# Optimization experiments

Measured on AMD Instinct MI355X. Metric: run time of the kernel, lower is better.

The kernel has to match this reference:

```python
import jax, jax.numpy as jnp
import numpy as np

H = 512      # hidden_size
NH = 8       # num_heads
DH = H // NH # head_dim = 64
NL = 2       # num_layers
R = 64       # number of AST relation types
PAD = 0      # padding relation index
FF = 4 * H   # FFN inner dim
B, T, S = 4, 512, 512
NEG = -1e10
EPS = 1e-5


def layer_norm(x, g, b):
    m = jnp.mean(x, axis=-1, keepdims=True)
    v = jnp.mean((x - m) ** 2, axis=-1, keepdims=True)
    return (x - m) * jax.lax.rsqrt(v + EPS) * g + b


def setup_inputs() -> dict:
    key = jax.random.key(0)
    ks = iter(jax.random.split(key, 40))

    def n(shape, scale=0.02):
        return jax.random.normal(next(ks), shape, dtype=jnp.float32) * scale

    inp = {
        'q': jax.random.normal(next(ks), (B, T, H), dtype=jnp.float32),
        'kv': jax.random.normal(next(ks), (B, S, H), dtype=jnp.float32),
        'rel_emb_k': n((R, DH)).at[PAD].set(0.0),
        'rel_emb_v': n((R, DH)).at[PAD].set(0.0),
        'Wq_s': n((NL, H, H)), 'bq_s': jnp.zeros((NL, H)),
        'Wk_s': n((NL, H, H)), 'Wv_s': n((NL, H, H)),
        'Wo_s': n((NL, H, H)), 'bo_s': jnp.zeros((NL, H)),
        'ln1_g': jnp.ones((NL, H)), 'ln1_b': jnp.zeros((NL, H)),
        'Wq_c': n((NL, H, H)), 'bq_c': jnp.zeros((NL, H)),
        'Wk_c': n((NL, H, H)), 'Wv_c': n((NL, H, H)),
        'Wo_c': n((NL, H, H)), 'bo_c': jnp.zeros((NL, H)),
        'ln2_g': jnp.ones((NL, H)), 'ln2_b': jnp.zeros((NL, H)),
        'W1': n((NL, H, FF)), 'b1': jnp.zeros((NL, FF)),
        'W2': n((NL, FF, H)), 'b2': jnp.zeros((NL, H)),
        'ln3_g': jnp.ones((NL, H)), 'ln3_b': jnp.zeros((NL, H)),
        'rel_ids': jax.random.randint(next(ks), (B, T, T), 0, R),
        'enc_mask': jnp.ones((B, S), dtype=bool),
    }
    return inp


def reference(q, kv, rel_emb_k, rel_emb_v,
              Wq_s, bq_s, Wk_s, Wv_s, Wo_s, bo_s, ln1_g, ln1_b,
              Wq_c, bq_c, Wk_c, Wv_c, Wo_c, bo_c, ln2_g, ln2_b,
              W1, b1, W2, b2, ln3_g, ln3_b,
              rel_ids, enc_mask):
    scale = np.sqrt(DH).astype(np.float32)
    # relation embeddings shared across layers/heads: [B,T,T,DH]
    rel_k = rel_emb_k[rel_ids]
    rel_v = rel_emb_v[rel_ids]
    tril = jnp.tril(jnp.ones((T, T), dtype=bool))
    rel_mask = (rel_ids != PAD) & tril[None]

    o = q
    for i in range(NL):
        # --- relation-aware masked self-attention ---
        Q = (o @ Wq_s[i] + bq_s[i]).reshape(B, T, NH, DH)
        K = (o @ Wk_s[i]).reshape(B, T, NH, DH)
        V = (o @ Wv_s[i]).reshape(B, T, NH, DH)
        # Q . (K + rel_k)^T decomposed to avoid materializing [B,NH,T,T,DH]
        e = (jnp.einsum('blhd,bmhd->bhlm', Q, K)
             + jnp.einsum('blhd,blmd->bhlm', Q, rel_k)) / scale
        e = jnp.where(rel_mask[:, None], e, NEG)
        a = jax.nn.softmax(e, axis=-1)
        att = (jnp.einsum('bhlm,bmhd->blhd', a, V)
               + jnp.einsum('bhlm,blmd->blhd', a, rel_v)).reshape(B, T, H)
        o = layer_norm(o + att @ Wo_s[i] + bo_s[i], ln1_g[i], ln1_b[i])

        # --- cross-attention ---
        Qc = (o @ Wq_c[i] + bq_c[i]).reshape(B, T, NH, DH)
        Kc = (kv @ Wk_c[i]).reshape(B, S, NH, DH)
        Vc = (kv @ Wv_c[i]).reshape(B, S, NH, DH)
        ec = jnp.einsum('bthd,bshd->bhts', Qc, Kc) / scale
        ec = jnp.where(enc_mask[:, None, None, :], ec, NEG)
        ac = jax.nn.softmax(ec, axis=-1)
        oc = jnp.einsum('bhts,bshd->bthd', ac, Vc).reshape(B, T, H)
        o = layer_norm(o + oc @ Wo_c[i] + bo_c[i], ln2_g[i], ln2_b[i])

        # --- feedforward ---
        h = jax.nn.relu(o @ W1[i] + b1[i])
        o = layer_norm(o + h @ W2[i] + b2[i], ln3_g[i], ln3_b[i])
    return o
```

## Files before the change

kernel.cpp:

```cpp
#include <hip/hip_runtime.h>

static constexpr int Hc  = 512;
static constexpr int NHc = 8;
static constexpr int DHc = 64;
static constexpr int NLc = 2;
static constexpr int Rc  = 64;
static constexpr int FFc = 2048;
static constexpr int Bc  = 4;
static constexpr int Tc  = 512;
#define NEGV (-1e10f)
#define EPSV 1e-5f
#define THRV 6.0f

typedef unsigned short u16;
typedef unsigned char u8;
typedef __attribute__((ext_vector_type(8))) short s16x8;
typedef __attribute__((ext_vector_type(4))) float f32x4;

__device__ __forceinline__ f32x4 mfma_bf16(s16x8 a, s16x8 b, f32x4 c) {
  return __builtin_amdgcn_mfma_f32_16x16x32_bf16(a, b, c, 0, 0, 0);
}
__device__ __forceinline__ u16 f2bf(float f) {
  union { float f; unsigned u; } x; x.f = f;
  unsigned r = (x.u + 0x7FFFu + ((x.u >> 16) & 1u)) >> 16;
  return (u16)r;
}
__device__ __forceinline__ float bf2f(u16 h) {
  union { unsigned u; float f; } x; x.u = ((unsigned)h) << 16;
  return x.f;
}
__device__ __forceinline__ unsigned cvtpk(float a, float b) {
  unsigned r;
  asm("v_cvt_pk_bf16_f32 %0, %1, %2" : "=v"(r) : "v"(a), "v"(b));
  return r;
}

template <int BM, int BN, bool RELU, int OUT>
__global__ __launch_bounds__(256) void gemm_mfma(
    const u16* __restrict__ A, const u16* __restrict__ Wt,
    const float* __restrict__ bias, int biasN,
    void* __restrict__ Cout, int N, int K) {
  __shared__ u16 As[BM * 32];
  __shared__ u16 Bs[BN * 32];
  const int tid = threadIdx.x;
  const int w = tid >> 6, lane = tid & 63, g = lane >> 4, li = lane & 15;
  const int bn = blockIdx.x * BN, bm = blockIdx.y * BM;
  const int r0 = (w & 1) * (BM / 2), c0 = (w >> 1) * (BN / 2);
  constexpr int MR = BM / 32, NR = BN / 32;
  constexpr int AIT = BM / 64, BIT = BN / 64;
  f32x4 acc[MR][NR];
#pragma unroll
  for (int i = 0; i < MR; ++i)
#pragma unroll
    for (int j = 0; j < NR; ++j) acc[i][j] = (f32x4){0.f, 0.f, 0.f, 0.f};

  s16x8 va[AIT], vb[BIT];
#pragma unroll
  for (int it = 0; it < AIT; ++it) {
    int s = it * 256 + tid, row = s >> 2, ch = s & 3;
    va[it] = *(const s16x8*)(A + (size_t)(bm + row) * K + ch * 8);
  }
#pragma unroll
  for (int it = 0; it < BIT; ++it) {
    int s = it * 256 + tid, row = s >> 2, ch = s & 3;
    vb[it] = *(const s16x8*)(Wt + (size_t)(bn + row) * K + ch * 8);
  }

  for (int k0 = 0; k0 < K; k0 += 32) {
    __syncthreads();
#pragma unroll
    for (int it = 0; it < AIT; ++it) {
      int s = it * 256 + tid, row = s >> 2, ch = s & 3;
      *(s16x8*)&As[row * 32 + ((ch ^ (row & 3)) * 8)] = va[it];
    }
#pragma unroll
    for (int it = 0; it < BIT; ++it) {
      int s = it * 256 + tid, row = s >> 2, ch = s & 3;
      *(s16x8*)&Bs[row * 32 + ((ch ^ (row & 3)) * 8)] = vb[it];
    }
    if (k0 + 32 < K) {
#pragma unroll
      for (int it = 0; it < AIT; ++it) {
        int s = it * 256 + tid, row = s >> 2, ch = s & 3;
        va[it] = *(const s16x8*)(A + (size_t)(bm + row) * K + k0 + 32 + ch * 8);
      }
#pragma unroll
      for (int it = 0; it < BIT; ++it) {
        int s = it * 256 + tid, row = s >> 2, ch = s & 3;
        vb[it] = *(const s16x8*)(Wt + (size_t)(bn + row) * K + k0 + 32 + ch * 8);
      }
    }
    __syncthreads();
    s16x8 ar[MR], br[NR];
#pragma unroll
    for (int i = 0; i < MR; ++i) {
      int row = r0 + i * 16 + li;
      ar[i] = *(const s16x8*)&As[row * 32 + ((g ^ (row & 3)) * 8)];
    }
#pragma unroll
    for (int j = 0; j < NR; ++j) {
      int row = c0 + j * 16 + li;
      br[j] = *(const s16x8*)&Bs[row * 32 + ((g ^ (row & 3)) * 8)];
    }
#pragma unroll
    for (int i = 0; i < MR; ++i)
#pragma unroll
      for (int j = 0; j < NR; ++j) acc[i][j] = mfma_bf16(ar[i], br[j], acc[i][j]);
  }

#pragma unroll
  for (int j = 0; j < NR; ++j) {
    int col = bn + c0 + j * 16 + li;
    float bv = (bias && col < biasN) ? bias[col] : 0.f;
#pragma unroll
    for (int i = 0; i < MR; ++i) {
#pragma unroll
      for (int r = 0; r < 4; ++r) {
        int rowg = bm + r0 + i * 16 + 4 * g + r;
        float v = acc[i][j][r] + bv;
        if (RELU) v = fmaxf(v, 0.f);
        if (OUT == 0) ((float*)Cout)[(size_t)rowg * N + col] = v;
        else          ((u16*)Cout)[(size_t)rowg * N + col] = f2bf(v);
      }
    }
  }
}

struct WPtrs { const float* p[10]; };

__global__ __launch_bounds__(256) void wcvt(WPtrs wp, u16* __restrict__ dst) {
  constexpr int NE = 20;
  constexpr int srcIdx[NE] = {0,1,0,1,3,3,4,4,5,5,6,6,7,7,2,2,8,8,9,9};
  constexpr int srcOff[NE] = {0,0,262144,262144,0,262144,0,262144,0,262144,
                              0,262144,0,262144,0,262144,0,1048576,0,1048576};
  constexpr int dstOff[NE] = {0,262144,524288,786432,1048576,1310720,
                              1572864,1835008,2097152,2359296,2621440,2883584,
                              3145728,3407872,3670016,3932160,
                              4194304,5242880,6291456,7340032};
  constexpr int KsA[NE] = {512,512,512,512,512,512,512,512,512,512,
                           512,512,512,512,512,512,512,512,2048,2048};
  constexpr int NsA[NE] = {512,512,512,512,512,512,512,512,512,512,
                           512,512,512,512,512,512,2048,2048,512,512};
  constexpr int tileStart[NE] = {0,64,128,192,256,320,384,448,512,576,
                                 640,704,768,832,896,960,1024,1280,1536,1792};
  __shared__ float ts[64 * 65];
  const int tid = threadIdx.x;
  const int bid = blockIdx.x;
  int e = 0;
#pragma unroll
  for (int i = 1; i < NE; ++i) if (bid >= tileStart[i]) e = i;
  const int t = bid - tileStart[e];
  const int Ks_ = KsA[e], Ns_ = NsA[e];
  const int tn = t % (Ns_ >> 6), tk = t / (Ns_ >> 6);
  const float* src = wp.p[srcIdx[e]] + srcOff[e];

  {
    int r = tid >> 2, cb = (tid & 3) * 16;
    const float* sp = src + (size_t)(tk * 64 + r) * Ns_ + tn * 64 + cb;
#pragma unroll
    for (int j = 0; j < 4; ++j) {
      float4 v = ((const float4*)sp)[j];
      float* d = &ts[r * 65 + cb + j * 4];
      d[0] = v.x; d[1] = v.y; d[2] = v.z; d[3] = v.w;
    }
  }
  __syncthreads();
  {
    int n = tid >> 2, kb = (tid & 3) * 16;
    u16* dp = dst + dstOff[e] + (size_t)(tn * 64 + n) * Ks_ + tk * 64 + kb;
    s16x8 o0, o1;
#pragma unroll
    for (int j = 0; j < 8; ++j) o0[j] = (short)f2bf(ts[(kb + j) * 65 + n]);
#pragma unroll
    for (int j = 0; j < 8; ++j) o1[j] = (short)f2bf(ts[(kb + 8 + j) * 65 + n]);
    *(s16x8*)dp = o0;
    *(s16x8*)(dp + 8) = o1;
  }
}

__global__ __launch_bounds__(256) void acvt(
    const float* __restrict__ q, const float* __restrict__ kv,
    const float* __restrict__ relv, const int* __restrict__ rel,
    u16* __restrict__ obf, u16* __restrict__ kvbf, u16* __restrict__ relvt,
    u8* __restrict__ rel8) {
  int bid = blockIdx.x, tid = threadIdx.x;
  if (bid >= 1025) {
    size_t i = (size_t)(bid - 1025) * 2048 + (size_t)tid * 8;
    int4 a = *(const int4*)(rel + i);
    int4 b = *(const int4*)(rel + i + 4);
    unsigned lo = (unsigned)(a.x & 255) | ((unsigned)(a.y & 255) << 8) |
                  ((unsigned)(a.z & 255) << 16) | ((unsigned)(a.w & 255) << 24);
    unsigned hi = (unsigned)(b.x & 255) | ((unsigned)(b.y & 255) << 8) |
                  ((unsigned)(b.z & 255) << 16) | ((unsigned)(b.w & 255) << 24);
    *(uint2*)(rel8 + i) = make_uint2(lo, hi);
    return;
  }
  if (bid == 1024) {
    int d = tid >> 2, rb = (tid & 3) * 16;
    s16x8 o0, o1;
#pragma unroll
    for (int j = 0; j < 8; ++j) o0[j] = (short)f2bf(relv[(rb + j) * 64 + d]);
#pragma unroll
    for (int j = 0; j < 8; ++j) o1[j] = (short)f2bf(relv[(rb + 8 + j) * 64 + d]);
    *(s16x8*)(relvt + d * 64 + rb) = o0;
    *(s16x8*)(relvt + d * 64 + rb + 8) = o1;
    return;
  }
  int i = bid * 256 + tid;
  const float* src; u16* dst; size_t off;
  if (i < 131072) { src = q; dst = obf; off = (size_t)i * 8; }
  else { src = kv; dst = kvbf; off = (size_t)(i - 131072) * 8; }
  float4 a = *(const float4*)(src + off);
  float4 b = *(const float4*)(src + off + 4);
  s16x8 o;
  o[0] = (short)f2bf(a.x); o[1] = (short)f2bf(a.y);
  o[2] = (short)f2bf(a.z); o[3] = (short)f2bf(a.w);
  o[4] = (short)f2bf(b.x); o[5] = (short)f2bf(b.y);
  o[6] = (short)f2bf(b.z); o[7] = (short)f2bf(b.w);
  *(s16x8*)(dst + off) = o;
}

__global__ __launch_bounds__(256) void qr_kernel(
    const u16* __restrict__ Q, const float* __restrict__ relk,
    u16* __restrict__ Qr) {
  __shared__ float rk[64 * 65];
  __shared__ float qs[4][64];
  const int tid = threadIdx.x;
  {
    int r = tid >> 2, cb = (tid & 3) * 16;
    const float* sp = relk + r * 64 + cb;
#pragma unroll
    for (int j = 0; j < 4; ++j) {
      float4 v = ((const float4*)sp)[j];
      float* d = &rk[r * 65 + cb + j * 4];
      d[0] = v.x; d[1] = v.y; d[2] = v.z; d[3] = v.w;
    }
  }
  const int sub = tid >> 6, r = tid & 63;
  const int unit = blockIdx.x * 4 + sub;
  qs[sub][r] = bf2f(Q[(size_t)(unit >> 3) * 1024 + (unit & 7) * 64 + r]);
  __syncthreads();
  float acc = 0.f;
#pragma unroll
  for (int d = 0; d < 64; ++d) acc += qs[sub][d] * rk[r * 65 + d];
  Qr[(size_t)unit * 64 + r] = f2bf(acc);
}

#define LOADKREL(KF, RF, C8) do {                                              \
    _Pragma("unroll") for (int mt = 0; mt < 4; ++mt) {                         \
      KF[mt * 2 + 0] = *(const s16x8*)(kp + (size_t)(C8) * 65536 + mt * 16384);\
      KF[mt * 2 + 1] = *(const s16x8*)(kp + (size_t)(C8) * 65536 + mt * 16384 + 32); \
      RF[mt] = *(const unsigned*)(rp8 + (C8) * 64 + mt * 16);                  \
    } } while (0)

#define COMPUTE_SELF(KF, RF, C8) do {                                          \
    s16x8 vf[8];                                                               \
    _Pragma("unroll") for (int df = 0; df < 4; ++df) {                         \
      vf[df * 2 + 0] = *(const s16x8*)(vp + (size_t)(C8) * 64 + df * 32768);   \
      vf[df * 2 + 1] = *(const s16x8*)(vp + (size_t)(C8) * 64 + df * 32768 + 32); } \
    f32x4 sf[4];                                                               \
    _Pragma("unroll") for (int mt = 0; mt < 4; ++mt) {                         \
      sf[mt] = (f32x4){0.f, 0.f, 0.f, 0.f};                                    \
      sf[mt] = mfma_bf16(KF[mt * 2 + 0], aq0, sf[mt]);                         \
      sf[mt] = mfma_bf16(KF[mt * 2 + 1], aq1, sf[mt]); }                       \
    float p[4][4];                                                             \
    int rl[4][4];                                                              \
    float pmax = NEGV;                                                         \
    _Pragma("unroll") for (int mt = 0; mt < 4; ++mt) {                         \
      _Pragma("unroll") for (int r = 0; r < 4; ++r) {                          \
        int rel = (int)((RF[mt] >> (8 * r)) & 255u);                           \
        rl[mt][r] = rel;                                                       \
        bool valid = (rel != 0) && ((C8) * 64 + mt * 16 + 4 * g + r <= lrow);  \
        p[mt][r] = valid ? (sf[mt][r] + qrs[li * 66 + rel]) * 0.125f : NEGV;   \
        pmax = fmaxf(pmax, p[mt][r]); } }                                      \
    pmax = fmaxf(pmax, __shfl_xor(pmax, 16));                                  \
    pmax = fmaxf(pmax, __shfl_xor(pmax, 32));                                  \
    if (__any(pmax > mrow + THRV)) {                                           \
      float mnew = (pmax > mrow + THRV) ? pmax : mrow;                         \
      float f = __expf(mrow - mnew);                                           \
      rsum *= f;                                                               \
      _Pragma("unroll") for (int j = 0; j < 8; ++j) {                          \
        float2* p2 = (float2*)&bk[li * 66 + g * 16 + 2 * j];                   \
        float2 v = *p2; v.x *= f; v.y *= f; *p2 = v; }                         \
      _Pragma("unroll") for (int r = 0; r < 4; ++r) {                          \
        float fr = __shfl(f, 4 * g + r);                                       \
        _Pragma("unroll") for (int df = 0; df < 4; ++df) oacc[df][r] *= fr; }  \
      mrow = mnew; }                                                           \
    unsigned pk[4][2];                                                         \
    _Pragma("unroll") for (int mt = 0; mt < 4; ++mt) {                         \
      _Pragma("unroll") for (int r = 0; r < 4; ++r) {                          \
        float pv = __expf(p[mt][r] - mrow);                                    \
        p[mt][r] = pv;                                                         \
        rsum += pv;                                                            \
        if (pv > 0.f) atomicAdd(&bk[li * 66 + rl[mt][r]], pv); }               \
      pk[mt][0] = cvtpk(p[mt][0], p[mt][1]);                                   \
      pk[mt][1] = cvtpk(p[mt][2], p[mt][3]); }                                 \
    _Pragma("unroll") for (int kk = 0; kk < 2; ++kk) {                         \
      union { s16x8 v; unsigned u[4]; } pa;                                    \
      _Pragma("unroll") for (int q = 0; q < 4; ++q) {                          \
        int src = ((2 * (g & 1) + (q >> 1)) << 4) + li;                        \
        unsigned uA = __shfl(pk[2 * kk][q & 1], src);                          \
        unsigned uB = __shfl(pk[2 * kk + 1][q & 1], src);                      \
        pa.u[q] = (g < 2) ? uA : uB; }                                         \
      _Pragma("unroll") for (int df = 0; df < 4; ++df)                         \
        oacc[df] = mfma_bf16(pa.v, vf[df * 2 + kk], oacc[df]); }               \
  } while (0)

__global__ __launch_bounds__(64) void attn_self_part(
    const u16* __restrict__ Qb, const u16* __restrict__ Kb,
    const u16* __restrict__ VT,
    const u16* __restrict__ Qrb, const u8* __restrict__ rel8,
    const u16* __restrict__ relvt,
    float* __restrict__ po, float2* __restrict__ pms) {
  __shared__ float qrs[16 * 66];
  __shared__ float buck[16 * 66];
  float* bk = buck;

  const int lane = threadIdx.x;
  const int g = lane >> 4, li = lane & 15;
  const int qt = blockIdx.x, h = blockIdx.y;
  const int b = blockIdx.z >> 2, s = blockIdx.z & 3;
  const int lrow = qt * 16 + li;
  const int growq = b * 512 + qt * 16;

  const u16* qp = Qb + (size_t)(growq + li) * 1024 + h * 64;
  s16x8 aq0 = *(const s16x8*)(qp + g * 8);
  s16x8 aq1 = *(const s16x8*)(qp + 32 + g * 8);
  const u16* kp = Kb + (size_t)(b * 512 + li) * 1024 + h * 64 + g * 8;
  const u16* vp = VT + (size_t)(h * 64 + li) * 2048 + b * 512 + g * 8;
  const u8* rp8 = rel8 + (size_t)(growq + li) * 512 + 4 * g;

  {
    int row = lane >> 2, c16 = (lane & 3) * 16;
    const u16* qrp = Qrb + ((size_t)(growq + row) * 8 + h) * 64 + c16;
    s16x8 v0 = *(const s16x8*)qrp;
    s16x8 v1 = *(const s16x8*)(qrp + 8);
#pragma unroll
    for (int j = 0; j < 8; ++j) {
      qrs[row * 66 + c16 + j] = bf2f((u16)v0[j]);
      qrs[row * 66 + c16 + 8 + j] = bf2f((u16)v1[j]);
    }
#pragma unroll
    for (int j = 0; j < 5; ++j) {
      int fid = j * 64 + lane;
      if (fid < 264) *(float4*)&buck[fid * 4] = make_float4(0.f, 0.f, 0.f, 0.f);
    }
  }

  float mrow = NEGV, rsum = 0.f;
  f32x4 oacc[4];
#pragma unroll
  for (int d = 0; d < 4; ++d) oacc[d] = (f32x4){0.f, 0.f, 0.f, 0.f};

  s16x8 kA[8], kB[8];
  unsigned rA[4], rB[4];
  LOADKREL(kA, rA, 2 * s);
  LOADKREL(kB, rB, 2 * s + 1);
  COMPUTE_SELF(kA, rA, 2 * s);
  COMPUTE_SELF(kB, rB, 2 * s + 1);

  rsum += __shfl_xor(rsum, 16);
  rsum += __shfl_xor(rsum, 32);

#pragma unroll
  for (int kk = 0; kk < 2; ++kk) {
    float bb[8];
#pragma unroll
    for (int j = 0; j < 4; ++j) {
      float2 v = *(const float2*)&bk[li * 66 + kk * 32 + g * 8 + 2 * j];
      bb[2 * j] = v.x; bb[2 * j + 1] = v.y;
    }
    union { s16x8 v; unsigned u[4]; } pb;
#pragma unroll
    for (int q = 0; q < 4; ++q) pb.u[q] = cvtpk(bb[2 * q], bb[2 * q + 1]);
#pragma unroll
    for (int df = 0; df < 4; ++df) {
      s16x8 rb = *(const s16x8*)(relvt + (df * 16 + li) * 64 + kk * 32 + g * 8);
      oacc[df] = mfma_bf16(pb.v, rb, oacc[df]);
    }
  }

  const size_t idx = (size_t)(b * 8 + h) * 512 + qt * 16;
#pragma unroll
  for (int df = 0; df < 4; ++df)
#pragma unroll
    for (int r = 0; r < 4; ++r)
      po[((idx + 4 * g + r) * 4 + s) * 64 + df * 16 + li] = oacc[df][r];
  if (lane < 16) pms[(idx + lane) * 4 + s] = make_float2(mrow, rsum);
}

#define LOADK_X(KF, C8) do {                                                   \
    _Pragma("unroll") for (int mt = 0; mt < 4; ++mt) {                         \
      KF[mt * 2 + 0] = *(const s16x8*)(kp + (size_t)(C8) * 65536 + mt * 16384);\
      KF[mt * 2 + 1] = *(const s16x8*)(kp + (size_t)(C8) * 65536 + mt * 16384 + 32); \
    } } while (0)

#define COMPUTE_X(KF, C8) do {                                                 \
    s16x8 vf[8];                                                               \
    _Pragma("unroll") for (int df = 0; df < 4; ++df) {                         \
      vf[df * 2 + 0] = *(const s16x8*)(vp + (size_t)(C8) * 64 + df * 32768);   \
      vf[df * 2 + 1] = *(const s16x8*)(vp + (size_t)(C8) * 64 + df * 32768 + 32); } \
    f32x4 sf[4];                                                               \
    _Pragma("unroll") for (int mt = 0; mt < 4; ++mt) {                         \
      sf[mt] = (f32x4){0.f, 0.f, 0.f, 0.f};                                    \
      sf[mt] = mfma_bf16(KF[mt * 2 + 0], aq0, sf[mt]);                         \
      sf[mt] = mfma_bf16(KF[mt * 2 + 1], aq1, sf[mt]); }                       \
    float p[4][4];                                                             \
    float pmax = NEGV;                                                         \
    _Pragma("unroll") for (int mt = 0; mt < 4; ++mt)                           \
      _Pragma("unroll") for (int r = 0; r < 4; ++r) {                          \
        p[mt][r] = sf[mt][r] * 0.125f;                                         \
        pmax = fmaxf(pmax, p[mt][r]); }                                        \
    pmax = fmaxf(pmax, __shfl_xor(pmax, 16));                                  \
    pmax = fmaxf(pmax, __shfl_xor(pmax, 32));                                  \
    if (__any(pmax > mrow + THRV)) {                                           \
      float mnew = (pmax > mrow + THRV) ? pmax : mrow;                         \
      float f = __expf(mrow - mnew);                                           \
      rsum *= f;                                                               \
      _Pragma("unroll") for (int r = 0; r < 4; ++r) {                          \
        float fr = __shfl(f, 4 * g + r);                                       \
        _Pragma("unroll") for (int df = 0; df < 4; ++df) oacc[df][r] *= fr; }  \
      mrow = mnew; }                                                           \
    unsigned pk[4][2];                                                         \
    _Pragma("unroll") for (int mt = 0; mt < 4; ++mt) {                         \
      _Pragma("unroll") for (int r = 0; r < 4; ++r) {                          \
        float pv = __expf(p[mt][r] - mrow);                                    \
        p[mt][r] = pv;                                                         \
        rsum += pv; }                                                          \
      pk[mt][0] = cvtpk(p[mt][0], p[mt][1]);                                   \
      pk[mt][1] = cvtpk(p[mt][2], p[mt][3]); }                                 \
    _Pragma("unroll") for (int kk = 0; kk < 2; ++kk) {                         \
      union { s16x8 v; unsigned u[4]; } pa;                                    \
      _Pragma("unroll") for (int q = 0; q < 4; ++q) {                          \
        int src = ((2 * (g & 1) + (q >> 1)) << 4) + li;                        \
        unsigned uA = __shfl(pk[2 * kk][q & 1], src);                          \
        unsigned uB = __shfl(pk[2 * kk + 1][q & 1], src);                      \
        pa.u[q] = (g < 2) ? uA : uB; }                                         \
      _Pragma("unroll") for (int df = 0; df < 4; ++df)                         \
        oacc[df] = mfma_bf16(pa.v, vf[df * 2 + kk], oacc[df]); }               \
  } while (0)

__global__ __launch_bounds__(64) void attn_cross_part(
    const u16* __restrict__ Qb,
    const u16* __restrict__ Kb,
    const u16* __restrict__ VT,
    float* __restrict__ po, float2* __restrict__ pms) {
  const int lane = threadIdx.x;
  const int g = lane >> 4, li = lane & 15;
  const int qt = blockIdx.x, h = blockIdx.y;
  const int b = blockIdx.z >> 2, s = blockIdx.z & 3;
  const int growq = b * 512 + qt * 16;

  const u16* qp = Qb + (size_t)(growq + li) * 512 + h * 64;
  s16x8 aq0 = *(const s16x8*)(qp + g * 8);
  s16x8 aq1 = *(const s16x8*)(qp + 32 + g * 8);
  const u16* kp = Kb + (size_t)(b * 512 + li) * 1024 + h * 64 + g * 8;
  const u16* vp = VT + (size_t)(h * 64 + li) * 2048 + b * 512 + g * 8;

  float mrow = NEGV, rsum = 0.f;
  f32x4 oacc[4];
#pragma unroll
  for (int d = 0; d < 4; ++d) oacc[d] = (f32x4){0.f, 0.f, 0.f, 0.f};

  s16x8 kA[8], kB[8];
  LOADK_X(kA, 2 * s);
  LOADK_X(kB, 2 * s + 1);
  COMPUTE_X(kA, 2 * s);
  COMPUTE_X(kB, 2 * s + 1);

  rsum += __shfl_xor(rsum, 16);
  rsum += __shfl_xor(rsum, 32);

  const size_t idx = (size_t)(b * 8 + h) * 512 + qt * 16;
#pragma unroll
  for (int df = 0; df < 4; ++df)
#pragma unroll
    for (int r = 0; r < 4; ++r)
      po[((idx + 4 * g + r) * 4 + s) * 64 + df * 16 + li] = oacc[df][r];
  if (lane < 16) pms[(idx + lane) * 4 + s] = make_float2(mrow, rsum);
}

__global__ __launch_bounds__(256) void attn_merge(
    const float* __restrict__ po, const float2* __restrict__ pms,
    u16* __restrict__ att) {
  const int t = threadIdx.x;
  const size_t idx = (size_t)blockIdx.x * 16 + (t >> 4);
  const int d4 = (t & 15) * 4;
  float2 ms[4];
  float m = NEGV;
#pragma unroll
  for (int s = 0; s < 4; ++s) {
    ms[s] = pms[idx * 4 + s];
    m = fmaxf(m, ms[s].x);
  }
  float rs = 0.f;
  float4 o = make_float4(0.f, 0.f, 0.f, 0.f);
#pragma unroll
  for (int s = 0; s < 4; ++s) {
    float f = __expf(ms[s].x - m);
    rs += f * ms[s].y;
    float4 v = *(const float4*)(po + (idx * 4 + s) * 64 + d4);
    o.x += f * v.x; o.y += f * v.y; o.z += f * v.z; o.w += f * v.w;
  }
  const float inv = 1.f / rs;
  const int b = (int)(idx >> 12), h = (int)(idx >> 9) & 7, row = (int)(idx & 511);
  ushort4 ov;
  ov.x = f2bf(o.x * inv);
  ov.y = f2bf(o.y * inv);
  ov.z = f2bf(o.z * inv);
  ov.w = f2bf(o.w * inv);
  *(ushort4*)(att + (size_t)(b * 512 + row) * 512 + h * 64 + d4) = ov;
}

__global__ __launch_bounds__(256) void ln_res(
    const float* __restrict__ x, const float* __restrict__ dlt,
    const float* __restrict__ g, const float* __restrict__ bta,
    float* __restrict__ out, u16* __restrict__ obf) {
  __shared__ float red_s[256];
  const int row = blockIdx.x, tid = threadIdx.x;
  const size_t base = (size_t)row * Hc;
  float v0 = x[base + tid] + dlt[base + tid];
  float v1 = x[base + tid + 256] + dlt[base + tid + 256];

  red_s[tid] = v0 + v1;
  __syncthreads();
  for (int s = 128; s > 0; s >>= 1) {
    if (tid < s) red_s[tid] += red_s[tid + s];
    __syncthreads();
  }
  const float mean = red_s[0] * (1.f / Hc);
  __syncthreads();
  const float d0 = v0 - mean, d1 = v1 - mean;
  red_s[tid] = d0 * d0 + d1 * d1;
  __syncthreads();
  for (int s = 128; s > 0; s >>= 1) {
    if (tid < s) red_s[tid] += red_s[tid + s];
    __syncthreads();
  }
  const float rstd = rsqrtf(red_s[0] * (1.f / Hc) + EPSV);
  float o0 = d0 * rstd * g[tid] + bta[tid];
  float o1 = d1 * rstd * g[tid + 256] + bta[tid + 256];
  out[base + tid] = o0;
  out[base + tid + 256] = o1;
  obf[base + tid] = f2bf(o0);
  obf[base + tid + 256] = f2bf(o1);
}

extern "C" void kernel_launch(void* const* d_in, const int* in_sizes, int n_in,
                              void* d_out, int out_size, void* d_ws, size_t ws_size,
                              hipStream_t stream) {
  const float* q    = (const float*)d_in[0];
  const float* kv   = (const float*)d_in[1];
  const float* relk = (const float*)d_in[2];
  const float* relv = (const float*)d_in[3];
  const float* Wq_s = (const float*)d_in[4];
  const float* bq_s = (const float*)d_in[5];
  const float* Wk_s = (const float*)d_in[6];
  const float* Wv_s = (const float*)d_in[7];
  const float* Wo_s = (const float*)d_in[8];
  const float* bo_s = (const float*)d_in[9];
  const float* ln1g = (const float*)d_in[10];
  const float* ln1b = (const float*)d_in[11];
  const float* Wq_c = (const float*)d_in[12];
  const float* bq_c = (const float*)d_in[13];
  const float* Wk_c = (const float*)d_in[14];
  const float* Wv_c = (const float*)d_in[15];
  const float* Wo_c = (const float*)d_in[16];
  const float* bo_c = (const float*)d_in[17];
  const float* ln2g = (const float*)d_in[18];
  const float* ln2b = (const float*)d_in[19];
  const float* W1   = (const float*)d_in[20];
  const float* b1   = (const float*)d_in[21];
  const float* W2   = (const float*)d_in[22];
  const float* b2   = (const float*)d_in[23];
  const float* ln3g = (const float*)d_in[24];
  const float* ln3b = (const float*)d_in[25];
  const int*   rel  = (const int*)d_in[26];

  char* wsb = (char*)d_ws;
  const size_t NT = (size_t)Bc * Tc;
  float* o     = (float*)wsb;  wsb += NT * Hc * 4;
  float* bDlt  = (float*)wsb;  wsb += NT * Hc * 4;
  u16* Qr      = (u16*)wsb;    wsb += NT * 8 * 64 * 2;
  u16* obf     = (u16*)wsb;    wsb += NT * Hc * 2;
  u16* kvbf    = (u16*)wsb;    wsb += NT * Hc * 2;
  u16* bQK     = (u16*)wsb;    wsb += NT * 1024 * 2;
  u16* bVt     = (u16*)wsb;    wsb += (size_t)512 * 2048 * 2;
  u16* bQc     = (u16*)wsb;    wsb += NT * Hc * 2;
  u16* bKc     = (u16*)wsb;    wsb += NT * 1024 * 2;
  u16* bVtc    = (u16*)wsb;    wsb += (size_t)1024 * 2048 * 2;
  u16* bAtt    = (u16*)wsb;    wsb += NT * Hc * 2;
  u16* bH      = (u16*)wsb;    wsb += NT * FFc * 2;
  u16* relvt   = (u16*)wsb;    wsb += 64 * 64 * 2;
  u8* rel8     = (u8*)wsb;     wsb += (size_t)NT * 512;
  u16* wbuf    = (u16*)wsb;    wsb += (size_t)8388608 * 2;
  float* po    = (float*)wsb;  wsb += (size_t)16384 * 4 * 64 * 4;
  float2* pms  = (float2*)wsb; wsb += (size_t)16384 * 4 * 8;

  WPtrs wp;
  wp.p[0] = Wq_s; wp.p[1] = Wk_s; wp.p[2] = Wv_s; wp.p[3] = Wo_s;
  wp.p[4] = Wq_c; wp.p[5] = Wk_c; wp.p[6] = Wv_c; wp.p[7] = Wo_c;
  wp.p[8] = W1;   wp.p[9] = W2;

  dim3 blk(256);
  wcvt<<<dim3(2048), blk, 0, stream>>>(wp, wbuf);
  acvt<<<dim3(1537), blk, 0, stream>>>(q, kv, relv, rel, obf, kvbf, relvt, rel8);
  hipMemcpyAsync(o, q, NT * Hc * 4, hipMemcpyDeviceToDevice, stream);

  gemm_mfma<64, 128, false, 1><<<dim3(8, 32), blk, 0, stream>>>(
      kvbf, wbuf + 2097152, nullptr, 0, bKc, 1024, 512);
  gemm_mfma<64, 128, false, 1><<<dim3(16, 16), blk, 0, stream>>>(
      wbuf + 2621440, kvbf, nullptr, 0, bVtc, 2048, 512);

  const dim3 gLN(NT);
  const dim3 gPART(32, 8, 16);
  const dim3 gMERGE(1024);
  for (int i = 0; i < NLc; ++i) {
    gemm_mfma<64, 128, false, 1><<<dim3(8, 32), blk, 0, stream>>>(
        obf, wbuf + (size_t)i * 524288, bq_s + i * Hc, Hc, bQK, 1024, 512);
    gemm_mfma<64, 64, false, 1><<<dim3(32, 8), blk, 0, stream>>>(
        wbuf + 3670016 + (size_t)i * 262144, obf, nullptr, 0, bVt, 2048, 512);
    qr_kernel<<<dim3(4096), blk, 0, stream>>>(bQK, relk, Qr);
    attn_self_part<<<gPART, dim3(64), 0, stream>>>(
        bQK, bQK + 512, bVt, Qr, rel8, relvt, po, pms);
    attn_merge<<<gMERGE, blk, 0, stream>>>(po, pms, bAtt);
    gemm_mfma<64, 64, false, 0><<<dim3(8, 32), blk, 0, stream>>>(
        bAtt, wbuf + 1048576 + (size_t)i * 262144, bo_s + i * Hc, Hc, bDlt, Hc, 512);
    ln_res<<<gLN, blk, 0, stream>>>(o, bDlt, ln1g + i * Hc, ln1b + i * Hc, o, obf);

    gemm_mfma<64, 64, false, 1><<<dim3(8, 32), blk, 0, stream>>>(
        obf, wbuf + 1572864 + (size_t)i * 262144, bq_c + i * Hc, Hc, bQc, Hc, 512);
    attn_cross_part<<<gPART, dim3(64), 0, stream>>>(
        bQc, bKc + i * 512, bVtc + (size_t)i * 512 * 2048, po, pms);
    attn_merge<<<gMERGE, blk, 0, stream>>>(po, pms, bAtt);
    gemm_mfma<64, 64, false, 0><<<dim3(8, 32), blk, 0, stream>>>(
        bAtt, wbuf + 3145728 + (size_t)i * 262144, bo_c + i * Hc, Hc, bDlt, Hc, 512);
    ln_res<<<gLN, blk, 0, stream>>>(o, bDlt, ln2g + i * Hc, ln2b + i * Hc, o, obf);

    gemm_mfma<64, 128, true, 1><<<dim3(16, 32), blk, 0, stream>>>(
        obf, wbuf + 4194304 + (size_t)i * 1048576, b1 + i * FFc, FFc, bH, FFc, 512);
    gemm_mfma<64, 64, false, 0><<<dim3(8, 32), blk, 0, stream>>>(
        bH, wbuf + 6291456 + (size_t)i * 1048576, b2 + i * Hc, Hc, bDlt, Hc, 2048);
    float* lnout = (i == NLc - 1) ? (float*)d_out : o;
    ln_res<<<gLN, blk, 0, stream>>>(o, bDlt, ln3g + i * Hc, ln3b + i * Hc, lnout, obf);
  }
}
```

Before: 389.4 us.

## Replace split-K flash attention with materialized score, softmax, and PV kernels

Replaces the fused online-softmax attention kernels (split across four key chunks with a merge pass) with three separate kernels: an MFMA score GEMM that writes bf16 scores to global memory, a row-wise softmax kernel that also builds the relation-value bucket sums, and a PV GEMM that folds the relation bucket in as extra K columns. The q-to-o fp32 copy is also fused into the input conversion kernel instead of using a separate memcpy. This removes the lazy-rescale logic, the per-element LDS atomics inside the MFMA loop, and the partial-result merge, at the cost of writing and reading full score and probability matrices through HBM and storing scores in bf16 before softmax.

```diff
diff --git a/kernel.cpp b/kernel.cpp
--- a/kernel.cpp
+++ b/kernel.cpp
@@ -10,7 +10,6 @@
 static constexpr int Tc  = 512;
 #define NEGV (-1e10f)
 #define EPSV 1e-5f
-#define THRV 6.0f
 
 typedef unsigned short u16;
 typedef unsigned char u8;
@@ -28,11 +27,6 @@
 __device__ __forceinline__ float bf2f(u16 h) {
   union { unsigned u; float f; } x; x.u = ((unsigned)h) << 16;
   return x.f;
-}
-__device__ __forceinline__ unsigned cvtpk(float a, float b) {
-  unsigned r;
-  asm("v_cvt_pk_bf16_f32 %0, %1, %2" : "=v"(r) : "v"(a), "v"(b));
-  return r;
 }
 
 template <int BM, int BN, bool RELU, int OUT>
@@ -182,7 +176,7 @@
     const float* __restrict__ q, const float* __restrict__ kv,
     const float* __restrict__ relv, const int* __restrict__ rel,
     u16* __restrict__ obf, u16* __restrict__ kvbf, u16* __restrict__ relvt,
-    u8* __restrict__ rel8) {
+    u8* __restrict__ rel8, float* __restrict__ ocp) {
   int bid = blockIdx.x, tid = threadIdx.x;
   if (bid >= 1025) {
     size_t i = (size_t)(bid - 1025) * 2048 + (size_t)tid * 8;
@@ -208,10 +202,15 @@
   }
   int i = bid * 256 + tid;
   const float* src; u16* dst; size_t off;
-  if (i < 131072) { src = q; dst = obf; off = (size_t)i * 8; }
+  bool isq = (i < 131072);
+  if (isq) { src = q; dst = obf; off = (size_t)i * 8; }
   else { src = kv; dst = kvbf; off = (size_t)(i - 131072) * 8; }
   float4 a = *(const float4*)(src + off);
   float4 b = *(const float4*)(src + off + 4);
+  if (isq) {
+    *(float4*)(ocp + off) = a;
+    *(float4*)(ocp + off + 4) = b;
+  }
   s16x8 o;
   o[0] = (short)f2bf(a.x); o[1] = (short)f2bf(a.y);
   o[2] = (short)f2bf(a.z); o[3] = (short)f2bf(a.w);
@@ -246,270 +245,181 @@
   Qr[(size_t)unit * 64 + r] = f2bf(acc);
 }
 
-#define LOADKREL(KF, RF, C8) do {                                              \
-    _Pragma("unroll") for (int mt = 0; mt < 4; ++mt) {                         \
-      KF[mt * 2 + 0] = *(const s16x8*)(kp + (size_t)(C8) * 65536 + mt * 16384);\
-      KF[mt * 2 + 1] = *(const s16x8*)(kp + (size_t)(C8) * 65536 + mt * 16384 + 32); \
-      RF[mt] = *(const unsigned*)(rp8 + (C8) * 64 + mt * 16);                  \
-    } } while (0)
-
-#define COMPUTE_SELF(KF, RF, C8) do {                                          \
-    s16x8 vf[8];                                                               \
-    _Pragma("unroll") for (int df = 0; df < 4; ++df) {                         \
-      vf[df * 2 + 0] = *(const s16x8*)(vp + (size_t)(C8) * 64 + df * 32768);   \
-      vf[df * 2 + 1] = *(const s16x8*)(vp + (size_t)(C8) * 64 + df * 32768 + 32); } \
-    f32x4 sf[4];                                                               \
-    _Pragma("unroll") for (int mt = 0; mt < 4; ++mt) {                         \
-      sf[mt] = (f32x4){0.f, 0.f, 0.f, 0.f};                                    \
-      sf[mt] = mfma_bf16(KF[mt * 2 + 0], aq0, sf[mt]);                         \
-      sf[mt] = mfma_bf16(KF[mt * 2 + 1], aq1, sf[mt]); }                       \
-    float p[4][4];                                                             \
-    int rl[4][4];                                                              \
-    float pmax = NEGV;                                                         \
-    _Pragma("unroll") for (int mt = 0; mt < 4; ++mt) {                         \
-      _Pragma("unroll") for (int r = 0; r < 4; ++r) {                          \
-        int rel = (int)((RF[mt] >> (8 * r)) & 255u);                           \
-        rl[mt][r] = rel;                                                       \
-        bool valid = (rel != 0) && ((C8) * 64 + mt * 16 + 4 * g + r <= lrow);  \
-        p[mt][r] = valid ? (sf[mt][r] + qrs[li * 66 + rel]) * 0.125f : NEGV;   \
-        pmax = fmaxf(pmax, p[mt][r]); } }                                      \
-    pmax = fmaxf(pmax, __shfl_xor(pmax, 16));                                  \
-    pmax = fmaxf(pmax, __shfl_xor(pmax, 32));                                  \
-    if (__any(pmax > mrow + THRV)) {                                           \
-      float mnew = (pmax > mrow + THRV) ? pmax : mrow;                         \
-      float f = __expf(mrow - mnew);                                           \
-      rsum *= f;                                                               \
-      _Pragma("unroll") for (int j = 0; j < 8; ++j) {                          \
-        float2* p2 = (float2*)&bk[li * 66 + g * 16 + 2 * j];                   \
-        float2 v = *p2; v.x *= f; v.y *= f; *p2 = v; }                         \
-      _Pragma("unroll") for (int r = 0; r < 4; ++r) {                          \
-        float fr = __shfl(f, 4 * g + r);                                       \
-        _Pragma("unroll") for (int df = 0; df < 4; ++df) oacc[df][r] *= fr; }  \
-      mrow = mnew; }                                                           \
-    unsigned pk[4][2];                                                         \
-    _Pragma("unroll") for (int mt = 0; mt < 4; ++mt) {                         \
-      _Pragma("unroll") for (int r = 0; r < 4; ++r) {                          \
-        float pv = __expf(p[mt][r] - mrow);                                    \
-        p[mt][r] = pv;                                                         \
-        rsum += pv;                                                            \
-        if (pv > 0.f) atomicAdd(&bk[li * 66 + rl[mt][r]], pv); }               \
-      pk[mt][0] = cvtpk(p[mt][0], p[mt][1]);                                   \
-      pk[mt][1] = cvtpk(p[mt][2], p[mt][3]); }                                 \
-    _Pragma("unroll") for (int kk = 0; kk < 2; ++kk) {                         \
-      union { s16x8 v; unsigned u[4]; } pa;                                    \
-      _Pragma("unroll") for (int q = 0; q < 4; ++q) {                          \
-        int src = ((2 * (g & 1) + (q >> 1)) << 4) + li;                        \
-        unsigned uA = __shfl(pk[2 * kk][q & 1], src);                          \
-        unsigned uB = __shfl(pk[2 * kk + 1][q & 1], src);                      \
-        pa.u[q] = (g < 2) ? uA : uB; }                                         \
-      _Pragma("unroll") for (int df = 0; df < 4; ++df)                         \
-        oacc[df] = mfma_bf16(pa.v, vf[df * 2 + kk], oacc[df]); }               \
-  } while (0)
-
-__global__ __launch_bounds__(64) void attn_self_part(
-    const u16* __restrict__ Qb, const u16* __restrict__ Kb,
-    const u16* __restrict__ VT,
-    const u16* __restrict__ Qrb, const u8* __restrict__ rel8,
-    const u16* __restrict__ relvt,
-    float* __restrict__ po, float2* __restrict__ pms) {
-  __shared__ float qrs[16 * 66];
-  __shared__ float buck[16 * 66];
-  float* bk = buck;
-
-  const int lane = threadIdx.x;
-  const int g = lane >> 4, li = lane & 15;
-  const int qt = blockIdx.x, h = blockIdx.y;
-  const int b = blockIdx.z >> 2, s = blockIdx.z & 3;
-  const int lrow = qt * 16 + li;
-  const int growq = b * 512 + qt * 16;
-
-  const u16* qp = Qb + (size_t)(growq + li) * 1024 + h * 64;
-  s16x8 aq0 = *(const s16x8*)(qp + g * 8);
-  s16x8 aq1 = *(const s16x8*)(qp + 32 + g * 8);
-  const u16* kp = Kb + (size_t)(b * 512 + li) * 1024 + h * 64 + g * 8;
-  const u16* vp = VT + (size_t)(h * 64 + li) * 2048 + b * 512 + g * 8;
-  const u8* rp8 = rel8 + (size_t)(growq + li) * 512 + 4 * g;
-
-  {
-    int row = lane >> 2, c16 = (lane & 3) * 16;
-    const u16* qrp = Qrb + ((size_t)(growq + row) * 8 + h) * 64 + c16;
-    s16x8 v0 = *(const s16x8*)qrp;
-    s16x8 v1 = *(const s16x8*)(qrp + 8);
-#pragma unroll
-    for (int j = 0; j < 8; ++j) {
-      qrs[row * 66 + c16 + j] = bf2f((u16)v0[j]);
-      qrs[row * 66 + c16 + 8 + j] = bf2f((u16)v1[j]);
-    }
-#pragma unroll
-    for (int j = 0; j < 5; ++j) {
-      int fid = j * 64 + lane;
-      if (fid < 264) *(float4*)&buck[fid * 4] = make_float4(0.f, 0.f, 0.f, 0.f);
-    }
-  }
-
-  float mrow = NEGV, rsum = 0.f;
-  f32x4 oacc[4];
-#pragma unroll
-  for (int d = 0; d < 4; ++d) oacc[d] = (f32x4){0.f, 0.f, 0.f, 0.f};
-
-  s16x8 kA[8], kB[8];
-  unsigned rA[4], rB[4];
-  LOADKREL(kA, rA, 2 * s);
-  LOADKREL(kB, rB, 2 * s + 1);
-  COMPUTE_SELF(kA, rA, 2 * s);
-  COMPUTE_SELF(kB, rB, 2 * s + 1);
-
-  rsum += __shfl_xor(rsum, 16);
-  rsum += __shfl_xor(rsum, 32);
-
-#pragma unroll
-  for (int kk = 0; kk < 2; ++kk) {
-    float bb[8];
+__global__ __launch_bounds__(256) void attn_score(
+    const u16* __restrict__ Qb, int qstride,
+    const u16* __restrict__ Kb, int kstride,
+    u16* __restrict__ S) {
+  const int tid = threadIdx.x;
+  const int w = tid >> 6, lane = tid & 63, g = lane >> 4, li = lane & 15;
+  const int mt = blockIdx.x, lt = blockIdx.y, bh = blockIdx.z;
+  const int b = bh >> 3, h = bh & 7;
+  const int lbase = lt * 128 + (w & 1) * 64;
+  const int mbase = mt * 128 + (w >> 1) * 64;
+
+  s16x8 aq[4][2], bk[4][2];
+#pragma unroll
+  for (int i = 0; i < 4; ++i) {
+    const u16* qp = Qb + (size_t)(b * 512 + lbase + i * 16 + li) * qstride + h * 64;
+    aq[i][0] = *(const s16x8*)(qp + g * 8);
+    aq[i][1] = *(const s16x8*)(qp + 32 + g * 8);
+  }
+#pragma unroll
+  for (int j = 0; j < 4; ++j) {
+    const u16* kp = Kb + (size_t)(b * 512 + mbase + j * 16 + li) * kstride + h * 64;
+    bk[j][0] = *(const s16x8*)(kp + g * 8);
+    bk[j][1] = *(const s16x8*)(kp + 32 + g * 8);
+  }
+  f32x4 acc[4][4];
+#pragma unroll
+  for (int i = 0; i < 4; ++i)
 #pragma unroll
     for (int j = 0; j < 4; ++j) {
-      float2 v = *(const float2*)&bk[li * 66 + kk * 32 + g * 8 + 2 * j];
-      bb[2 * j] = v.x; bb[2 * j + 1] = v.y;
-    }
-    union { s16x8 v; unsigned u[4]; } pb;
-#pragma unroll
-    for (int q = 0; q < 4; ++q) pb.u[q] = cvtpk(bb[2 * q], bb[2 * q + 1]);
-#pragma unroll
-    for (int df = 0; df < 4; ++df) {
-      s16x8 rb = *(const s16x8*)(relvt + (df * 16 + li) * 64 + kk * 32 + g * 8);
-      oacc[df] = mfma_bf16(pb.v, rb, oacc[df]);
-    }
-  }
-
-  const size_t idx = (size_t)(b * 8 + h) * 512 + qt * 16;
-#pragma unroll
-  for (int df = 0; df < 4; ++df)
-#pragma unroll
-    for (int r = 0; r < 4; ++r)
-      po[((idx + 4 * g + r) * 4 + s) * 64 + df * 16 + li] = oacc[df][r];
-  if (lane < 16) pms[(idx + lane) * 4 + s] = make_float2(mrow, rsum);
-}
-
-#define LOADK_X(KF, C8) do {                                                   \
-    _Pragma("unroll") for (int mt = 0; mt < 4; ++mt) {                         \
-      KF[mt * 2 + 0] = *(const s16x8*)(kp + (size_t)(C8) * 65536 + mt * 16384);\
-      KF[mt * 2 + 1] = *(const s16x8*)(kp + (size_t)(C8) * 65536 + mt * 16384 + 32); \
-    } } while (0)
-
-#define COMPUTE_X(KF, C8) do {                                                 \
-    s16x8 vf[8];                                                               \
-    _Pragma("unroll") for (int df = 0; df < 4; ++df) {                         \
-      vf[df * 2 + 0] = *(const s16x8*)(vp + (size_t)(C8) * 64 + df * 32768);   \
-      vf[df * 2 + 1] = *(const s16x8*)(vp + (size_t)(C8) * 64 + df * 32768 + 32); } \
-    f32x4 sf[4];                                                               \
-    _Pragma("unroll") for (int mt = 0; mt < 4; ++mt) {                         \
-      sf[mt] = (f32x4){0.f, 0.f, 0.f, 0.f};                                    \
-      sf[mt] = mfma_bf16(KF[mt * 2 + 0], aq0, sf[mt]);                         \
-      sf[mt] = mfma_bf16(KF[mt * 2 + 1], aq1, sf[mt]); }                       \
-    float p[4][4];                                                             \
-    float pmax = NEGV;                                                         \
-    _Pragma("unroll") for (int mt = 0; mt < 4; ++mt)                           \
-      _Pragma("unroll") for (int r = 0; r < 4; ++r) {                          \
-        p[mt][r] = sf[mt][r] * 0.125f;                                         \
-        pmax = fmaxf(pmax, p[mt][r]); }                                        \
-    pmax = fmaxf(pmax, __shfl_xor(pmax, 16));                                  \
-    pmax = fmaxf(pmax, __shfl_xor(pmax, 32));                                  \
-    if (__any(pmax > mrow + THRV)) {                                           \
-      float mnew = (pmax > mrow + THRV) ? pmax : mrow;                         \
-      float f = __expf(mrow - mnew);                                           \
-      rsum *= f;                                                               \
-      _Pragma("unroll") for (int r = 0; r < 4; ++r) {                          \
-        float fr = __shfl(f, 4 * g + r);                                       \
-        _Pragma("unroll") for (int df = 0; df < 4; ++df) oacc[df][r] *= fr; }  \
-      mrow = mnew; }                                                           \
-    unsigned pk[4][2];                                                         \
-    _Pragma("unroll") for (int mt = 0; mt < 4; ++mt) {                         \
-      _Pragma("unroll") for (int r = 0; r < 4; ++r) {                          \
-        float pv = __expf(p[mt][r] - mrow);                                    \
-        p[mt][r] = pv;                                                         \
-        rsum += pv; }                                                          \
-      pk[mt][0] = cvtpk(p[mt][0], p[mt][1]);                                   \
-      pk[mt][1] = cvtpk(p[mt][2], p[mt][3]); }                                 \
-    _Pragma("unroll") for (int kk = 0; kk < 2; ++kk) {                         \
-      union { s16x8 v; unsigned u[4]; } pa;                                    \
-      _Pragma("unroll") for (int q = 0; q < 4; ++q) {                          \
-        int src = ((2 * (g & 1) + (q >> 1)) << 4) + li;                        \
-        unsigned uA = __shfl(pk[2 * kk][q & 1], src);                          \
-        unsigned uB = __shfl(pk[2 * kk + 1][q & 1], src);                      \
-        pa.u[q] = (g < 2) ? uA : uB; }                                         \
-      _Pragma("unroll") for (int df = 0; df < 4; ++df)                         \
-        oacc[df] = mfma_bf16(pa.v, vf[df * 2 + kk], oacc[df]); }               \
-  } while (0)
-
-__global__ __launch_bounds__(64) void attn_cross_part(
-    const u16* __restrict__ Qb,
-    const u16* __restrict__ Kb,
-    const u16* __restrict__ VT,
-    float* __restrict__ po, float2* __restrict__ pms) {
-  const int lane = threadIdx.x;
-  const int g = lane >> 4, li = lane & 15;
-  const int qt = blockIdx.x, h = blockIdx.y;
-  const int b = blockIdx.z >> 2, s = blockIdx.z & 3;
-  const int growq = b * 512 + qt * 16;
-
-  const u16* qp = Qb + (size_t)(growq + li) * 512 + h * 64;
-  s16x8 aq0 = *(const s16x8*)(qp + g * 8);
-  s16x8 aq1 = *(const s16x8*)(qp + 32 + g * 8);
-  const u16* kp = Kb + (size_t)(b * 512 + li) * 1024 + h * 64 + g * 8;
-  const u16* vp = VT + (size_t)(h * 64 + li) * 2048 + b * 512 + g * 8;
-
-  float mrow = NEGV, rsum = 0.f;
-  f32x4 oacc[4];
-#pragma unroll
-  for (int d = 0; d < 4; ++d) oacc[d] = (f32x4){0.f, 0.f, 0.f, 0.f};
-
-  s16x8 kA[8], kB[8];
-  LOADK_X(kA, 2 * s);
-  LOADK_X(kB, 2 * s + 1);
-  COMPUTE_X(kA, 2 * s);
-  COMPUTE_X(kB, 2 * s + 1);
-
-  rsum += __shfl_xor(rsum, 16);
-  rsum += __shfl_xor(rsum, 32);
-
-  const size_t idx = (size_t)(b * 8 + h) * 512 + qt * 16;
-#pragma unroll
-  for (int df = 0; df < 4; ++df)
-#pragma unroll
-    for (int r = 0; r < 4; ++r)
-      po[((idx + 4 * g + r) * 4 + s) * 64 + df * 16 + li] = oacc[df][r];
-  if (lane < 16) pms[(idx + lane) * 4 + s] = make_float2(mrow, rsum);
-}
-
-__global__ __launch_bounds__(256) void attn_merge(
-    const float* __restrict__ po, const float2* __restrict__ pms,
-    u16* __restrict__ att) {
-  const int t = threadIdx.x;
-  const size_t idx = (size_t)blockIdx.x * 16 + (t >> 4);
-  const int d4 = (t & 15) * 4;
-  float2 ms[4];
-  float m = NEGV;
-#pragma unroll
-  for (int s = 0; s < 4; ++s) {
-    ms[s] = pms[idx * 4 + s];
-    m = fmaxf(m, ms[s].x);
-  }
-  float rs = 0.f;
-  float4 o = make_float4(0.f, 0.f, 0.f, 0.f);
-#pragma unroll
-  for (int s = 0; s < 4; ++s) {
-    float f = __expf(ms[s].x - m);
-    rs += f * ms[s].y;
-    float4 v = *(const float4*)(po + (idx * 4 + s) * 64 + d4);
-    o.x += f * v.x; o.y += f * v.y; o.z += f * v.z; o.w += f * v.w;
-  }
+      acc[i][j] = mfma_bf16(aq[i][0], bk[j][0], (f32x4){0.f, 0.f, 0.f, 0.f});
+      acc[i][j] = mfma_bf16(aq[i][1], bk[j][1], acc[i][j]);
+    }
+  u16* Sb = S + (size_t)bh * 262144;
+#pragma unroll
+  for (int j = 0; j < 4; ++j)
+#pragma unroll
+    for (int i = 0; i < 4; ++i)
+#pragma unroll
+      for (int r = 0; r < 4; ++r)
+        Sb[(size_t)(lbase + i * 16 + 4 * g + r) * 512 + mbase + j * 16 + li] =
+            f2bf(acc[i][j][r]);
+}
+
+__global__ __launch_bounds__(256) void attn_smax_self(
+    const u16* __restrict__ S, const u8* __restrict__ rel8,
+    const u16* __restrict__ Qrb, u16* __restrict__ P) {
+  __shared__ float qrs[4][64];
+  __shared__ float buck[4][64];
+  const int tid = threadIdx.x;
+  const int w = tid >> 6, lane = tid & 63;
+  const int rowid = blockIdx.x * 4 + w;
+  const int bh = rowid >> 9, l = rowid & 511;
+  const int b = bh >> 3, h = bh & 7;
+
+  qrs[w][lane] = bf2f(Qrb[((size_t)(b * 512 + l) * 8 + h) * 64 + lane]);
+  buck[w][lane] = 0.f;
+
+  s16x8 sv = *(const s16x8*)(S + (size_t)bh * 262144 + (size_t)l * 512 + lane * 8);
+  uint2 rv = *(const uint2*)(rel8 + (size_t)(b * 512 + l) * 512 + (size_t)lane * 8);
+  int rl[8];
+#pragma unroll
+  for (int j = 0; j < 4; ++j) rl[j] = (int)((rv.x >> (8 * j)) & 255u);
+#pragma unroll
+  for (int j = 0; j < 4; ++j) rl[4 + j] = (int)((rv.y >> (8 * j)) & 255u);
+
+  float e[8];
+  float mx = NEGV;
+#pragma unroll
+  for (int j = 0; j < 8; ++j) {
+    int m = lane * 8 + j;
+    bool valid = (rl[j] != 0) && (m <= l);
+    e[j] = valid ? (bf2f((u16)sv[j]) + qrs[w][rl[j]]) * 0.125f : NEGV;
+    mx = fmaxf(mx, e[j]);
+  }
+#pragma unroll
+  for (int msk = 1; msk < 64; msk <<= 1) mx = fmaxf(mx, __shfl_xor(mx, msk));
+
+  float p[8], rs = 0.f;
+#pragma unroll
+  for (int j = 0; j < 8; ++j) {
+    p[j] = __expf(e[j] - mx);
+    rs += p[j];
+    atomicAdd(&buck[w][rl[j]], p[j]);
+  }
+#pragma unroll
+  for (int msk = 1; msk < 64; msk <<= 1) rs += __shfl_xor(rs, msk);
   const float inv = 1.f / rs;
-  const int b = (int)(idx >> 12), h = (int)(idx >> 9) & 7, row = (int)(idx & 511);
-  ushort4 ov;
-  ov.x = f2bf(o.x * inv);
-  ov.y = f2bf(o.y * inv);
-  ov.z = f2bf(o.z * inv);
-  ov.w = f2bf(o.w * inv);
-  *(ushort4*)(att + (size_t)(b * 512 + row) * 512 + h * 64 + d4) = ov;
+
+  u16* Pr = P + (size_t)bh * 294912 + (size_t)l * 576;
+  s16x8 ov;
+#pragma unroll
+  for (int j = 0; j < 8; ++j) ov[j] = (short)f2bf(p[j] * inv);
+  *(s16x8*)(Pr + lane * 8) = ov;
+  Pr[512 + lane] = f2bf(buck[w][lane] * inv);
+}
+
+__global__ __launch_bounds__(256) void attn_smax_cross(
+    const u16* __restrict__ S, u16* __restrict__ P) {
+  const int tid = threadIdx.x;
+  const int w = tid >> 6, lane = tid & 63;
+  const int rowid = blockIdx.x * 4 + w;
+  const int bh = rowid >> 9, l = rowid & 511;
+
+  s16x8 sv = *(const s16x8*)(S + (size_t)bh * 262144 + (size_t)l * 512 + lane * 8);
+  float e[8];
+  float mx = NEGV;
+#pragma unroll
+  for (int j = 0; j < 8; ++j) {
+    e[j] = bf2f((u16)sv[j]) * 0.125f;
+    mx = fmaxf(mx, e[j]);
+  }
+#pragma unroll
+  for (int msk = 1; msk < 64; msk <<= 1) mx = fmaxf(mx, __shfl_xor(mx, msk));
+  float p[8], rs = 0.f;
+#pragma unroll
+  for (int j = 0; j < 8; ++j) {
+    p[j] = __expf(e[j] - mx);
+    rs += p[j];
+  }
+#pragma unroll
+  for (int msk = 1; msk < 64; msk <<= 1) rs += __shfl_xor(rs, msk);
+  const float inv = 1.f / rs;
+  u16* Pr = P + (size_t)bh * 294912 + (size_t)l * 576;
+  s16x8 ov;
+#pragma unroll
+  for (int j = 0; j < 8; ++j) ov[j] = (short)f2bf(p[j] * inv);
+  *(s16x8*)(Pr + lane * 8) = ov;
+}
+
+template <int KT>
+__global__ __launch_bounds__(256) void attn_pv(
+    const u16* __restrict__ P, const u16* __restrict__ VT, int vstride,
+    const u16* __restrict__ relvt, u16* __restrict__ att) {
+  const int tid = threadIdx.x;
+  const int w = tid >> 6, lane = tid & 63, g = lane >> 4, li = lane & 15;
+  const int lt = blockIdx.x, bh = blockIdx.y;
+  const int b = bh >> 3, h = bh & 7;
+  const int r0 = (w & 1) * 32, c0 = (w >> 1) * 32;
+  const u16* Pb = P + (size_t)bh * 294912;
+
+  f32x4 acc[2][2];
+#pragma unroll
+  for (int i = 0; i < 2; ++i)
+#pragma unroll
+    for (int j = 0; j < 2; ++j) acc[i][j] = (f32x4){0.f, 0.f, 0.f, 0.f};
+
+  for (int k0 = 0; k0 < KT * 32; k0 += 32) {
+    s16x8 ar[2], br[2];
+#pragma unroll
+    for (int i = 0; i < 2; ++i) {
+      int l = lt * 64 + r0 + i * 16 + li;
+      ar[i] = *(const s16x8*)(Pb + (size_t)l * 576 + k0 + g * 8);
+    }
+#pragma unroll
+    for (int j = 0; j < 2; ++j) {
+      int n = c0 + j * 16 + li;
+      br[j] = (k0 < 512)
+          ? *(const s16x8*)(VT + (size_t)(h * 64 + n) * vstride + b * 512 + k0 + g * 8)
+          : *(const s16x8*)(relvt + n * 64 + (k0 - 512) + g * 8);
+    }
+#pragma unroll
+    for (int i = 0; i < 2; ++i)
+#pragma unroll
+      for (int j = 0; j < 2; ++j) acc[i][j] = mfma_bf16(ar[i], br[j], acc[i][j]);
+  }
+#pragma unroll
+  for (int i = 0; i < 2; ++i)
+#pragma unroll
+    for (int j = 0; j < 2; ++j)
+#pragma unroll
+      for (int r = 0; r < 4; ++r) {
+        int l = lt * 64 + r0 + i * 16 + 4 * g + r;
+        int d = c0 + j * 16 + li;
+        att[(size_t)(b * 512 + l) * 512 + h * 64 + d] = f2bf(acc[i][j][r]);
+      }
 }
 
 __global__ __launch_bounds__(256) void ln_res(
@@ -594,8 +504,8 @@
   u16* relvt   = (u16*)wsb;    wsb += 64 * 64 * 2;
   u8* rel8     = (u8*)wsb;     wsb += (size_t)NT * 512;
   u16* wbuf    = (u16*)wsb;    wsb += (size_t)8388608 * 2;
-  float* po    = (float*)wsb;  wsb += (size_t)16384 * 4 * 64 * 4;
-  float2* pms  = (float2*)wsb; wsb += (size_t)16384 * 4 * 8;
+  u16* S       = (u16*)wsb;    wsb += (size_t)32 * 262144 * 2;
+  u16* P       = (u16*)wsb;    wsb += (size_t)32 * 294912 * 2;
 
   WPtrs wp;
   wp.p[0] = Wq_s; wp.p[1] = Wk_s; wp.p[2] = Wv_s; wp.p[3] = Wo_s;
@@ -604,8 +514,8 @@
 
   dim3 blk(256);
   wcvt<<<dim3(2048), blk, 0, stream>>>(wp, wbuf);
-  acvt<<<dim3(1537), blk, 0, stream>>>(q, kv, relv, rel, obf, kvbf, relvt, rel8);
-  hipMemcpyAsync(o, q, NT * Hc * 4, hipMemcpyDeviceToDevice, stream);
+  acvt<<<dim3(1537), blk, 0, stream>>>(q, kv, relv, rel, obf, kvbf, relvt,
+                                       rel8, o);
 
   gemm_mfma<64, 128, false, 1><<<dim3(8, 32), blk, 0, stream>>>(
       kvbf, wbuf + 2097152, nullptr, 0, bKc, 1024, 512);
@@ -613,26 +523,28 @@
       wbuf + 2621440, kvbf, nullptr, 0, bVtc, 2048, 512);
 
   const dim3 gLN(NT);
-  const dim3 gPART(32, 8, 16);
-  const dim3 gMERGE(1024);
+  const dim3 gSC(4, 4, 32);
+  const dim3 gSM(4096);
+  const dim3 gPV(8, 32);
   for (int i = 0; i < NLc; ++i) {
     gemm_mfma<64, 128, false, 1><<<dim3(8, 32), blk, 0, stream>>>(
         obf, wbuf + (size_t)i * 524288, bq_s + i * Hc, Hc, bQK, 1024, 512);
     gemm_mfma<64, 64, false, 1><<<dim3(32, 8), blk, 0, stream>>>(
         wbuf + 3670016 + (size_t)i * 262144, obf, nullptr, 0, bVt, 2048, 512);
     qr_kernel<<<dim3(4096), blk, 0, stream>>>(bQK, relk, Qr);
-    attn_self_part<<<gPART, dim3(64), 0, stream>>>(
-        bQK, bQK + 512, bVt, Qr, rel8, relvt, po, pms);
-    attn_merge<<<gMERGE, blk, 0, stream>>>(po, pms, bAtt);
+    attn_score<<<gSC, blk, 0, stream>>>(bQK, 1024, bQK + 512, 1024, S);
+    attn_smax_self<<<gSM, blk, 0, stream>>>(S, rel8, Qr, P);
+    attn_pv<18><<<gPV, blk, 0, stream>>>(P, bVt, 2048, relvt, bAtt);
     gemm_mfma<64, 64, false, 0><<<dim3(8, 32), blk, 0, stream>>>(
         bAtt, wbuf + 1048576 + (size_t)i * 262144, bo_s + i * Hc, Hc, bDlt, Hc, 512);
     ln_res<<<gLN, blk, 0, stream>>>(o, bDlt, ln1g + i * Hc, ln1b + i * Hc, o, obf);
 
     gemm_mfma<64, 64, false, 1><<<dim3(8, 32), blk, 0, stream>>>(
         obf, wbuf + 1572864 + (size_t)i * 262144, bq_c + i * Hc, Hc, bQc, Hc, 512);
-    attn_cross_part<<<gPART, dim3(64), 0, stream>>>(
-        bQc, bKc + i * 512, bVtc + (size_t)i * 512 * 2048, po, pms);
-    attn_merge<<<gMERGE, blk, 0, stream>>>(po, pms, bAtt);
+    attn_score<<<gSC, blk, 0, stream>>>(bQc, 512, bKc + i * 512, 1024, S);
+    attn_smax_cross<<<gSM, blk, 0, stream>>>(S, P);
+    attn_pv<16><<<gPV, blk, 0, stream>>>(
+        P, bVtc + (size_t)i * 512 * 2048, 2048, relvt, bAtt);
     gemm_mfma<64, 64, false, 0><<<dim3(8, 32), blk, 0, stream>>>(
         bAtt, wbuf + 3145728 + (size_t)i * 262144, bo_c + i * Hc, Hc, bDlt, Hc, 512);
     ln_res<<<gLN, blk, 0, stream>>>(o, bDlt, ln2g + i * Hc, ln2b + i * Hc, o, obf);
```

Result: slower. 415.0 us (+6.6%).
